# Optimization experiments

Measured on AMD Instinct MI355X. Metric: run time of the kernel, lower is better.

Reference implementation:

```python
import jax, jax.numpy as jnp
from jax import lax
import numpy as np

B, L, M, D = 128, 1024, 68, 2
H = 256          # lstm hidden
IN = M * D       # 136
FF1, FF2 = 256, 512
NLAYERS = 3


def _p(key, shape, scale=0.05):
    return (jax.random.normal(key, shape, dtype=jnp.float32) * scale)


def setup_inputs() -> dict:
    key = jax.random.key(0)
    ks = jax.random.split(key, 20)
    inp = {
        "x": jax.random.normal(ks[0], (B, L, M, D), dtype=jnp.float32),
        "length": jax.random.randint(ks[1], (B,), 1, L + 1, dtype=jnp.int32),
        # MLP: Linear(136,256) -> ReLU -> Linear(256,512) -> ReLU
        "W1": _p(ks[2], (FF1, IN)), "b1": _p(ks[3], (FF1,)),
        "W2": _p(ks[4], (FF2, FF1)), "b2": _p(ks[5], (FF2,)),
        # 3-layer LSTM(512 -> 256), torch gate order i,f,g,o
        "w_ih0": _p(ks[6], (4 * H, FF2)), "w_hh0": _p(ks[7], (4 * H, H)),
        "b_ih0": _p(ks[8], (4 * H,)), "b_hh0": _p(ks[9], (4 * H,)),
        "w_ih1": _p(ks[10], (4 * H, H)), "w_hh1": _p(ks[11], (4 * H, H)),
        "b_ih1": _p(ks[12], (4 * H,)), "b_hh1": _p(ks[13], (4 * H,)),
        "w_ih2": _p(ks[14], (4 * H, H)), "w_hh2": _p(ks[15], (4 * H, H)),
        "b_ih2": _p(ks[16], (4 * H,)), "b_hh2": _p(ks[17], (4 * H,)),
        # decision head Linear(256, 1)
        "Wd": _p(ks[18], (1, H)), "bd": _p(ks[19], (1,)),
    }
    return inp


def lstm_layer(x, w_ih, w_hh, b_ih, b_hh):
    # x: [B, L, Din] -> [B, L, H]; zero initial (h, c)
    b, l, _ = x.shape
    h = w_hh.shape[1]
    xg = jnp.einsum('bld,gd->blg', x, w_ih) + b_ih + b_hh  # [B,L,4H]
    xg = jnp.swapaxes(xg, 0, 1)  # [L,B,4H]

    def step(carry, xt):
        hh, cc = carry
        gates = xt + hh @ w_hh.T
        i, f, g, o = jnp.split(gates, 4, axis=-1)
        i = jax.nn.sigmoid(i)
        f = jax.nn.sigmoid(f)
        g = jnp.tanh(g)
        o = jax.nn.sigmoid(o)
        cc = f * cc + i * g
        hh = o * jnp.tanh(cc)
        return (hh, cc), hh

    init = (jnp.zeros((b, h), x.dtype), jnp.zeros((b, h), x.dtype))
    _, hs = lax.scan(step, init, xg)
    return jnp.swapaxes(hs, 0, 1)  # [B,L,H]


def reference(x, length, W1, b1, W2, b2,
              w_ih0, w_hh0, b_ih0, b_hh0,
              w_ih1, w_hh1, b_ih1, b_hh1,
              w_ih2, w_hh2, b_ih2, b_hh2,
              Wd, bd):
    b, l, m, d = x.shape
    feat = x.reshape(b, l, m * d)
    feat = jax.nn.relu(jnp.einsum('bld,od->blo', feat, W1) + b1)
    feat = jax.nn.relu(jnp.einsum('bld,od->blo', feat, W2) + b2)  # [B,L,512]
    h = lstm_layer(feat, w_ih0, w_hh0, b_ih0, b_hh0)
    h = lstm_layer(h, w_ih1, w_hh1, b_ih1, b_hh1)
    h = lstm_layer(h, w_ih2, w_hh2, b_ih2, b_hh2)  # [B,L,256]
    decision = jnp.einsum('blh,oh->blo', h, Wd)[..., 0] + bd[0]  # [B,L]
    # ragged mean over the first length[i] timesteps (AdaptiveAvgPool1d(1))
    mask = (jnp.arange(l)[None, :] < length[:, None]).astype(decision.dtype)
    out = jnp.sum(decision * mask, axis=1) / length.astype(decision.dtype)
    return out  # [B]
```

## Files before the change

### kernel.cpp

```cpp
#include <hip/hip_runtime.h>
#include <hip/hip_fp16.h>

#define TCH 256
#define NCH 4

typedef __attribute__((ext_vector_type(8))) _Float16 half8;
typedef __attribute__((ext_vector_type(2))) _Float16 half2v;
typedef __attribute__((ext_vector_type(4))) float floatx4;

__device__ __forceinline__ float dot2f(unsigned a, unsigned b, float c) {
#if __has_builtin(__builtin_amdgcn_fdot2)
  return __builtin_amdgcn_fdot2(__builtin_bit_cast(half2v, a),
                                __builtin_bit_cast(half2v, b), c, false);
#else
  __half2 x = __builtin_bit_cast(__half2, a);
  __half2 y = __builtin_bit_cast(__half2, b);
  c = fmaf(__half2float(x.x), __half2float(y.x), c);
  c = fmaf(__half2float(x.y), __half2float(y.y), c);
  return c;
#endif
}

template<bool AF32, bool RELUB>
__global__ __launch_bounds__(256, 2) void gemm_k(
    const void* __restrict__ Ab, const float* __restrict__ Bw,
    const float* __restrict__ bias, __half* __restrict__ C,
    const int* __restrict__ length, int K, int KT, int N, int arst, int t0)
{
  int b = blockIdx.x >> 1;
  int tloc0 = (blockIdx.x & 1) << 7;
  if (t0 + tloc0 >= length[b]) return;

  __shared__ half8 As[128][5];
  __shared__ half8 Bs[128][5];

  int tid = threadIdx.x;
  int wave = tid >> 6, lane = tid & 63;
  int wm = (wave & 1) << 6, wn = (wave >> 1) << 6;
  int quad = lane >> 4, sub = lane & 15;
  int n0 = blockIdx.y << 7;

  floatx4 acc[4][4];
#pragma unroll
  for (int i = 0; i < 4; ++i)
#pragma unroll
    for (int j = 0; j < 4; ++j)
#pragma unroll
      for (int e = 0; e < 4; ++e) acc[i][j][e] = 0.f;

  size_t arowbase = (size_t)b * arst + tloc0;

  for (int kt = 0; kt < KT; ++kt) {
    int k0 = kt << 5;
#pragma unroll
    for (int pass = 0; pass < 2; ++pass) {
      int idx = tid + (pass << 8);
      int r = idx >> 2, c8 = (idx & 3) << 3;
      int kb = k0 + c8;
      half8 v;
      if (AF32) {
        const float* src = (const float*)Ab + (arowbase + r) * K + kb;
        if (kb + 8 <= K) {
          float4 u0 = *(const float4*)(src);
          float4 u1 = *(const float4*)(src + 4);
          v[0] = (_Float16)u0.x; v[1] = (_Float16)u0.y; v[2] = (_Float16)u0.z; v[3] = (_Float16)u0.w;
          v[4] = (_Float16)u1.x; v[5] = (_Float16)u1.y; v[6] = (_Float16)u1.z; v[7] = (_Float16)u1.w;
        } else {
#pragma unroll
          for (int i = 0; i < 8; ++i) v[i] = (kb + i < K) ? (_Float16)src[i] : (_Float16)0.f;
        }
      } else {
        const __half* src = (const __half*)Ab + (arowbase + r) * K + kb;
        if (kb + 8 <= K) v = *(const half8*)src;
        else {
#pragma unroll
          for (int i = 0; i < 8; ++i) v[i] = (kb + i < K) ? *(const _Float16*)(src + i) : (_Float16)0.f;
        }
      }
      As[r][c8 >> 3] = v;
      const float* bsrc = Bw + (size_t)(n0 + r) * K + kb;
      half8 w;
      if (kb + 8 <= K) {
        float4 u0 = *(const float4*)(bsrc);
        float4 u1 = *(const float4*)(bsrc + 4);
        w[0] = (_Float16)u0.x; w[1] = (_Float16)u0.y; w[2] = (_Float16)u0.z; w[3] = (_Float16)u0.w;
        w[4] = (_Float16)u1.x; w[5] = (_Float16)u1.y; w[6] = (_Float16)u1.z; w[7] = (_Float16)u1.w;
      } else {
#pragma unroll
        for (int i = 0; i < 8; ++i) w[i] = (kb + i < K) ? (_Float16)bsrc[i] : (_Float16)0.f;
      }
      Bs[r][c8 >> 3] = w;
    }
    __syncthreads();
    half8 af[4], bf[4];
#pragma unroll
    for (int i = 0; i < 4; ++i) {
      af[i] = As[wm + (i << 4) + sub][quad];
      bf[i] = Bs[wn + (i << 4) + sub][quad];
    }
#pragma unroll
    for (int mt = 0; mt < 4; ++mt)
#pragma unroll
      for (int nt = 0; nt < 4; ++nt)
        acc[mt][nt] = __builtin_amdgcn_mfma_f32_16x16x32_f16(af[mt], bf[nt], acc[mt][nt], 0, 0, 0);
    __syncthreads();
  }
  size_t mrowbase = (size_t)blockIdx.x << 7;
#pragma unroll
  for (int nt = 0; nt < 4; ++nt) {
    int n = n0 + wn + (nt << 4) + sub;
    float bv = 0.f;
    if (RELUB) bv = bias[n];
#pragma unroll
    for (int mt = 0; mt < 4; ++mt) {
#pragma unroll
      for (int r4 = 0; r4 < 4; ++r4) {
        int m = wm + (mt << 4) + (quad << 2) + r4;
        float v = acc[mt][nt][r4] + bv;
        if (RELUB) v = fmaxf(v, 0.f);
        C[(mrowbase + m) * (size_t)N + n] = __float2half(v);
      }
    }
  }
}

__global__ __launch_bounds__(512, 2) void scan_k(
    const __half* __restrict__ xg, const float* __restrict__ whh,
    const float* __restrict__ bih, const float* __restrict__ bhh,
    __half* __restrict__ hout, unsigned* __restrict__ hstate,
    float* __restrict__ cstate, unsigned long long* __restrict__ exch,
    const int* __restrict__ length, int t0)
{
  int b = blockIdx.x >> 1, hf = blockIdx.x & 1;
  int len = length[b];
  int tend = min(t0 + TCH, len);
  if (t0 >= tend) return;

  int tid = threadIdx.x;
  int lane = tid & 63;
  int gate = tid >> 7, hl = tid & 127;
  int row = (gate << 8) + (hf << 7) + hl;

  __shared__ float gbuf[512];
  __shared__ unsigned short hbf[128];
  __shared__ unsigned opair[64];

  unsigned wp[128];
  {
    const float* wsrc = whh + (size_t)row * 256;
#pragma unroll
    for (int p2 = 0; p2 < 64; ++p2) {
      float4 f = *(const float4*)(wsrc + (p2 << 2));
      unsigned pk0 = ((unsigned)__half_as_ushort(__float2half(f.y)) << 16) | __half_as_ushort(__float2half(f.x));
      unsigned pk1 = ((unsigned)__half_as_ushort(__float2half(f.w)) << 16) | __half_as_ushort(__float2half(f.z));
      int p = p2 << 1;
      int pj0 = ((p >> 6) == hf) ? (p & 63) : (64 + (p & 63));
      int pa = p + 1;
      int pj1 = ((pa >> 6) == hf) ? (pa & 63) : (64 + (pa & 63));
      wp[pj0] = pk0;
      wp[pj1] = pk1;
    }
  }
  float biasr = bih[row] + bhh[row];

  unsigned hp0 = 0, hp1 = 0;
  float cv = 0.f;
  if (t0 > 0) {
    hp0 = hstate[(b << 7) + (hf << 6) + lane];
    hp1 = hstate[(b << 7) + ((1 - hf) << 6) + lane];
    if (tid < 128) cv = cstate[(b << 8) + (hf << 7) + tid];
  }

  const __half* xgp = xg + ((size_t)b * TCH) * 1024 + row;
  unsigned long long* exA = exch + ((((size_t)b << 1) | (size_t)hf) << 7);
  unsigned long long* exB = exch + ((((size_t)b << 1) | (size_t)(1 - hf)) << 7);

  for (int t = t0; t < tend; ++t) {
    float xgv = __half2float(xgp[(size_t)(t - t0) << 10]);
    float acc = biasr;
#pragma unroll
    for (int j = 0; j < 64; ++j)
      acc = dot2f(wp[j], (unsigned)__builtin_amdgcn_readlane(hp0, j), acc);
    if (t > t0) {
      const unsigned long long* pw = exB + ((t & 1) << 6) + lane;
      unsigned long long w = __hip_atomic_load(pw, __ATOMIC_RELAXED, __HIP_MEMORY_SCOPE_AGENT);
      while ((int)(unsigned)(w >> 32) != t) {
        __builtin_amdgcn_s_sleep(2);
        w = __hip_atomic_load(pw, __ATOMIC_RELAXED, __HIP_MEMORY_SCOPE_AGENT);
      }
      hp1 = (unsigned)w;
    }
#pragma unroll
    for (int j = 0; j < 64; ++j)
      acc = dot2f(wp[64 + j], (unsigned)__builtin_amdgcn_readlane(hp1, j), acc);
    acc += xgv;
    float gv = (gate == 2) ? tanhf(acc) : (1.f / (1.f + __expf(-acc)));
    gbuf[tid] = gv;
    __syncthreads();
    if (tid < 128) {
      float iv = gbuf[tid], fv = gbuf[128 + tid], gg = gbuf[256 + tid], ov = gbuf[384 + tid];
      cv = fv * cv + iv * gg;
      float hv = ov * tanhf(cv);
      __half hh = __float2half(hv);
      hout[(((size_t)b * TCH) + (t - t0)) * 256 + (hf << 7) + tid] = hh;
      hbf[tid] = __half_as_ushort(hh);
    }
    __syncthreads();
    if (tid < 64) {
      unsigned pr = ((unsigned)hbf[(tid << 1) + 1] << 16) | hbf[tid << 1];
      opair[tid] = pr;
      __hip_atomic_store(exA + (((t + 1) & 1) << 6) + tid,
                         ((unsigned long long)(unsigned)(t + 1) << 32) | (unsigned long long)pr,
                         __ATOMIC_RELAXED, __HIP_MEMORY_SCOPE_AGENT);
    }
    __syncthreads();
    hp0 = opair[lane];
  }
  if (tid < 64) hstate[(b << 7) + (hf << 6) + tid] = hp0;
  if (tid < 128) cstate[(b << 8) + (hf << 7) + tid] = cv;
}

__global__ __launch_bounds__(256, 2) void head_k(
    const __half* __restrict__ h2, const float* __restrict__ Wd,
    const float* __restrict__ bd, const int* __restrict__ length,
    float* __restrict__ dacc, float* __restrict__ out, int t0, int first, int last)
{
  int b = blockIdx.x, tid = threadIdx.x;
  int lane = tid & 63, wave = tid >> 6;
  int len = length[b];
  int tend = min(t0 + TCH, len);
  float4 w4 = *(const float4*)(Wd + (lane << 2));
  float wsum = 0.f;
  for (int t = t0 + wave; t < tend; t += 4) {
    const __half* hr = h2 + (((size_t)b * TCH) + (t - t0)) * 256 + (lane << 2);
    uint2 u = *(const uint2*)hr;
    __half2 p0 = __builtin_bit_cast(__half2, u.x);
    __half2 p1 = __builtin_bit_cast(__half2, u.y);
    float s = w4.x * __half2float(p0.x) + w4.y * __half2float(p0.y)
            + w4.z * __half2float(p1.x) + w4.w * __half2float(p1.y);
#pragma unroll
    for (int off = 32; off > 0; off >>= 1) s += __shfl_xor(s, off);
    wsum += s;
  }
  __shared__ float wred[4];
  if (lane == 0) wred[wave] = wsum;
  __syncthreads();
  if (tid == 0) {
    int cnt = tend - t0; if (cnt < 0) cnt = 0;
    float tot = wred[0] + wred[1] + wred[2] + wred[3] + bd[0] * (float)cnt;
    if (!first) tot += dacc[b];
    dacc[b] = tot;
    if (last) out[b] = tot / (float)len;
  }
}

extern "C" void kernel_launch(void* const* d_in, const int* in_sizes, int n_in,
                              void* d_out, int out_size, void* d_ws, size_t ws_size,
                              hipStream_t stream) {
  (void)in_sizes; (void)n_in; (void)out_size; (void)ws_size;
  const float* x    = (const float*)d_in[0];
  const int* length = (const int*)d_in[1];
  const float* W1   = (const float*)d_in[2];
  const float* b1   = (const float*)d_in[3];
  const float* W2   = (const float*)d_in[4];
  const float* b2   = (const float*)d_in[5];
  const float* wih[3] = {(const float*)d_in[6],  (const float*)d_in[10], (const float*)d_in[14]};
  const float* whh[3] = {(const float*)d_in[7],  (const float*)d_in[11], (const float*)d_in[15]};
  const float* bih[3] = {(const float*)d_in[8],  (const float*)d_in[12], (const float*)d_in[16]};
  const float* bhh[3] = {(const float*)d_in[9],  (const float*)d_in[13], (const float*)d_in[17]};
  const float* Wd   = (const float*)d_in[18];
  const float* bd   = (const float*)d_in[19];
  float* out = (float*)d_out;

  char* ws = (char*)d_ws;
  __half* XG    = (__half*)(ws);
  __half* FEAT1 = (__half*)(ws + 67108864);
  __half* FEAT2 = (__half*)(ws + 83886080);
  __half* HBUF  = (__half*)(ws + 117440512);
  unsigned* HST = (unsigned*)(ws + 134217728);
  float* CST    = (float*)(ws + 134217728 + 196608);
  unsigned long long* EXC = (unsigned long long*)(ws + 134217728 + 589824);
  float* DACC   = (float*)(ws + 134217728 + 589824 + 786432);

  for (int c = 0; c < NCH; ++c) {
    int t0 = c * TCH;
    gemm_k<true,  true ><<<dim3(256, 2), 256, 0, stream>>>(
        (const void*)(x + (size_t)t0 * 136), W1, b1, FEAT1, length, 136, 5, 256, 1024, t0);
    gemm_k<false, true ><<<dim3(256, 4), 256, 0, stream>>>(
        (const void*)FEAT1, W2, b2, FEAT2, length, 256, 8, 512, TCH, t0);
    gemm_k<false, false><<<dim3(256, 8), 256, 0, stream>>>(
        (const void*)FEAT2, wih[0], nullptr, XG, length, 512, 16, 1024, TCH, t0);
    scan_k<<<256, 512, 0, stream>>>(XG, whh[0], bih[0], bhh[0], HBUF,
                                    HST, CST, EXC, length, t0);
    gemm_k<false, false><<<dim3(256, 8), 256, 0, stream>>>(
        (const void*)HBUF, wih[1], nullptr, XG, length, 256, 8, 1024, TCH, t0);
    scan_k<<<256, 512, 0, stream>>>(XG, whh[1], bih[1], bhh[1], HBUF,
                                    HST + 16384, CST + 32768, EXC + 32768, length, t0);
    gemm_k<false, false><<<dim3(256, 8), 256, 0, stream>>>(
        (const void*)HBUF, wih[2], nullptr, XG, length, 256, 8, 1024, TCH, t0);
    scan_k<<<256, 512, 0, stream>>>(XG, whh[2], bih[2], bhh[2], HBUF,
                                    HST + 32768, CST + 65536, EXC + 65536, length, t0);
    head_k<<<128, 256, 0, stream>>>(HBUF, Wd, bd, length, DACC, out, t0, c == 0, c == NCH - 1);
  }
}
```

Before: 6.474 ms.

## Batch LSTM recurrence over 16 sequences per block using MFMA

Replaces the per-sequence scalar dot2 recurrence (two blocks per batch element, exchanging halves of h) with a kernel where groups of 16 batch rows are split across 8 blocks by hidden-column slice. Each step computes the recurrent matmul with 16x16x32 f16 MFMA. The full h vector is exchanged through tagged global slots that every block polls. This is meant to cut the serial per-step latency and the total block count. In exchange, each block now waits on 8 peer blocks per step and runs up to the longest sequence in its group. It also depends on all 64 blocks being co-resident to avoid deadlock.

After: 11.81 ms. 1.82x slower.

```diff
diff --git a/kernel.cpp b/kernel.cpp
--- a/kernel.cpp
+++ b/kernel.cpp
@@ -5,21 +5,7 @@
 #define NCH 4
 
 typedef __attribute__((ext_vector_type(8))) _Float16 half8;
-typedef __attribute__((ext_vector_type(2))) _Float16 half2v;
 typedef __attribute__((ext_vector_type(4))) float floatx4;
-
-__device__ __forceinline__ float dot2f(unsigned a, unsigned b, float c) {
-#if __has_builtin(__builtin_amdgcn_fdot2)
-  return __builtin_amdgcn_fdot2(__builtin_bit_cast(half2v, a),
-                                __builtin_bit_cast(half2v, b), c, false);
-#else
-  __half2 x = __builtin_bit_cast(__half2, a);
-  __half2 y = __builtin_bit_cast(__half2, b);
-  c = fmaf(__half2float(x.x), __half2float(y.x), c);
-  c = fmaf(__half2float(x.y), __half2float(y.y), c);
-  return c;
-#endif
-}
 
 template<bool AF32, bool RELUB>
 __global__ __launch_bounds__(256, 2) void gemm_k(
@@ -124,100 +110,132 @@
   }
 }
 
-__global__ __launch_bounds__(512, 2) void scan_k(
+__global__ __launch_bounds__(256, 2) void scan2_k(
     const __half* __restrict__ xg, const float* __restrict__ whh,
     const float* __restrict__ bih, const float* __restrict__ bhh,
-    __half* __restrict__ hout, unsigned* __restrict__ hstate,
-    float* __restrict__ cstate, unsigned long long* __restrict__ exch,
+    __half* __restrict__ hout, float* __restrict__ cstate,
+    unsigned long long* __restrict__ exch,
     const int* __restrict__ length, int t0)
 {
-  int b = blockIdx.x >> 1, hf = blockIdx.x & 1;
-  int len = length[b];
-  int tend = min(t0 + TCH, len);
+  const int g = blockIdx.x >> 3, s = blockIdx.x & 7;
+  const int b0 = g << 4;
+  int maxlen = 0;
+#pragma unroll
+  for (int i = 0; i < 16; ++i) maxlen = max(maxlen, length[b0 + i]);
+  const int tend = min(t0 + TCH, maxlen);
   if (t0 >= tend) return;
 
-  int tid = threadIdx.x;
-  int lane = tid & 63;
-  int gate = tid >> 7, hl = tid & 127;
-  int row = (gate << 8) + (hf << 7) + hl;
-
-  __shared__ float gbuf[512];
-  __shared__ unsigned short hbf[128];
-  __shared__ unsigned opair[64];
-
-  unsigned wp[128];
-  {
-    const float* wsrc = whh + (size_t)row * 256;
-#pragma unroll
-    for (int p2 = 0; p2 < 64; ++p2) {
-      float4 f = *(const float4*)(wsrc + (p2 << 2));
-      unsigned pk0 = ((unsigned)__half_as_ushort(__float2half(f.y)) << 16) | __half_as_ushort(__float2half(f.x));
-      unsigned pk1 = ((unsigned)__half_as_ushort(__float2half(f.w)) << 16) | __half_as_ushort(__float2half(f.z));
-      int p = p2 << 1;
-      int pj0 = ((p >> 6) == hf) ? (p & 63) : (64 + (p & 63));
-      int pa = p + 1;
-      int pj1 = ((pa >> 6) == hf) ? (pa & 63) : (64 + (pa & 63));
-      wp[pj0] = pk0;
-      wp[pj1] = pk1;
-    }
-  }
-  float biasr = bih[row] + bhh[row];
-
-  unsigned hp0 = 0, hp1 = 0;
-  float cv = 0.f;
-  if (t0 > 0) {
-    hp0 = hstate[(b << 7) + (hf << 6) + lane];
-    hp1 = hstate[(b << 7) + ((1 - hf) << 6) + lane];
-    if (tid < 128) cv = cstate[(b << 8) + (hf << 7) + tid];
-  }
-
-  const __half* xgp = xg + ((size_t)b * TCH) * 1024 + row;
-  unsigned long long* exA = exch + ((((size_t)b << 1) | (size_t)hf) << 7);
-  unsigned long long* exB = exch + ((((size_t)b << 1) | (size_t)(1 - hf)) << 7);
+  const int tid = threadIdx.x;
+  const int wave = tid >> 6, lane = tid & 63;
+  const int quad = lane >> 4, sub = lane & 15;
+
+  __shared__ __align__(16) __half h_lds[16][264];
+  __shared__ __align__(16) __half xgl[16][136];
+  __shared__ __align__(16) float gbuf[128][20];
+
+  half8 wB[8][2];
+  float bias2[2];
+#pragma unroll
+  for (int nt = 0; nt < 2; ++nt) {
+    int gcol = (wave << 8) + (s << 5) + (nt << 4) + sub;
+    bias2[nt] = bih[gcol] + bhh[gcol];
+#pragma unroll
+    for (int kt = 0; kt < 8; ++kt) {
+      const float* p = whh + (size_t)gcol * 256 + (kt << 5) + (quad << 3);
+      float4 a = *(const float4*)p;
+      float4 b4 = *(const float4*)(p + 4);
+      half8 v;
+      v[0] = (_Float16)a.x;  v[1] = (_Float16)a.y;  v[2] = (_Float16)a.z;  v[3] = (_Float16)a.w;
+      v[4] = (_Float16)b4.x; v[5] = (_Float16)b4.y; v[6] = (_Float16)b4.z; v[7] = (_Float16)b4.w;
+      wB[kt][nt] = v;
+    }
+  }
+
+  const int ub = tid >> 4, uc = tid & 15;
+  const int d0 = uc << 1;
+  float2 cc = make_float2(0.f, 0.f);
+  if (t0 > 0) cc = *(const float2*)&cstate[(size_t)((b0 + ub) << 8) + (s << 5) + d0];
+
+  if (t0 == 0) {
+    unsigned* hz = (unsigned*)&h_lds[0][0];
+    for (int i = tid; i < 16 * 132; i += 256) hz[i] = 0u;
+  }
+
+  const int sb = tid >> 4, sc = tid & 15;
+  const __half* xbase = xg + ((size_t)(b0 + sb) * TCH) * 1024
+                        + ((sc >> 2) << 8) + (s << 5) + ((sc & 3) << 3);
+  const unsigned long long* exrd = exch + ((size_t)(b0 + sb) << 1) * 128;
+  const size_t exwr_row = ((size_t)(b0 + ub) << 1);
+  const int widx = (s << 4) + uc;
 
   for (int t = t0; t < tend; ++t) {
-    float xgv = __half2float(xgp[(size_t)(t - t0) << 10]);
-    float acc = biasr;
-#pragma unroll
-    for (int j = 0; j < 64; ++j)
-      acc = dot2f(wp[j], (unsigned)__builtin_amdgcn_readlane(hp0, j), acc);
-    if (t > t0) {
-      const unsigned long long* pw = exB + ((t & 1) << 6) + lane;
-      unsigned long long w = __hip_atomic_load(pw, __ATOMIC_RELAXED, __HIP_MEMORY_SCOPE_AGENT);
-      while ((int)(unsigned)(w >> 32) != t) {
-        __builtin_amdgcn_s_sleep(2);
-        w = __hip_atomic_load(pw, __ATOMIC_RELAXED, __HIP_MEMORY_SCOPE_AGENT);
-      }
-      hp1 = (unsigned)w;
-    }
-#pragma unroll
-    for (int j = 0; j < 64; ++j)
-      acc = dot2f(wp[64 + j], (unsigned)__builtin_amdgcn_readlane(hp1, j), acc);
-    acc += xgv;
-    float gv = (gate == 2) ? tanhf(acc) : (1.f / (1.f + __expf(-acc)));
-    gbuf[tid] = gv;
+    const int tl = t - t0;
+    uint4 xv = *(const uint4*)(xbase + (size_t)tl * 1024);
+    if (t > 0) {
+      const unsigned long long* src = exrd + ((t & 1) << 7) + (sc << 3);
+      unsigned long long w[8];
+#pragma unroll
+      for (int j = 0; j < 8; ++j)
+        w[j] = __hip_atomic_load(src + j, __ATOMIC_RELAXED, __HIP_MEMORY_SCOPE_AGENT);
+      while (true) {
+        int bad = 0;
+#pragma unroll
+        for (int j = 0; j < 8; ++j) bad |= ((int)(unsigned)(w[j] >> 32) != t);
+        if (!bad) break;
+        __builtin_amdgcn_s_sleep(1);
+#pragma unroll
+        for (int j = 0; j < 8; ++j)
+          w[j] = __hip_atomic_load(src + j, __ATOMIC_RELAXED, __HIP_MEMORY_SCOPE_AGENT);
+      }
+      uint4 q0, q1;
+      q0.x = (unsigned)w[0]; q0.y = (unsigned)w[1]; q0.z = (unsigned)w[2]; q0.w = (unsigned)w[3];
+      q1.x = (unsigned)w[4]; q1.y = (unsigned)w[5]; q1.z = (unsigned)w[6]; q1.w = (unsigned)w[7];
+      *(uint4*)&h_lds[sb][(sc << 4)] = q0;
+      *(uint4*)&h_lds[sb][(sc << 4) + 8] = q1;
+    }
+    *(uint4*)&xgl[sb][((sc >> 2) << 5) + ((sc & 3) << 3)] = xv;
     __syncthreads();
-    if (tid < 128) {
-      float iv = gbuf[tid], fv = gbuf[128 + tid], gg = gbuf[256 + tid], ov = gbuf[384 + tid];
-      cv = fv * cv + iv * gg;
-      float hv = ov * tanhf(cv);
-      __half hh = __float2half(hv);
-      hout[(((size_t)b * TCH) + (t - t0)) * 256 + (hf << 7) + tid] = hh;
-      hbf[tid] = __half_as_ushort(hh);
+
+    floatx4 acc0 = {0.f, 0.f, 0.f, 0.f}, acc1 = {0.f, 0.f, 0.f, 0.f};
+#pragma unroll
+    for (int kt = 0; kt < 8; ++kt) {
+      half8 af = *(const half8*)&h_lds[sub][(kt << 5) + (quad << 3)];
+      acc0 = __builtin_amdgcn_mfma_f32_16x16x32_f16(af, wB[kt][0], acc0, 0, 0, 0);
+      acc1 = __builtin_amdgcn_mfma_f32_16x16x32_f16(af, wB[kt][1], acc1, 0, 0, 0);
+    }
+#pragma unroll
+    for (int nt = 0; nt < 2; ++nt) {
+      floatx4 av = nt ? acc1 : acc0;
+      float4 o;
+#pragma unroll
+      for (int r = 0; r < 4; ++r) {
+        float xvv = __half2float(xgl[(quad << 2) + r][(wave << 5) + (nt << 4) + sub]);
+        float pre = av[r] + xvv + bias2[nt];
+        float res;
+        if (wave == 2) res = tanhf(pre);
+        else           res = 1.f / (1.f + __expf(-pre));
+        (&o.x)[r] = res;
+      }
+      *(float4*)&gbuf[(wave << 5) + (nt << 4) + sub][quad << 2] = o;
     }
     __syncthreads();
-    if (tid < 64) {
-      unsigned pr = ((unsigned)hbf[(tid << 1) + 1] << 16) | hbf[tid << 1];
-      opair[tid] = pr;
-      __hip_atomic_store(exA + (((t + 1) & 1) << 6) + tid,
-                         ((unsigned long long)(unsigned)(t + 1) << 32) | (unsigned long long)pr,
-                         __ATOMIC_RELAXED, __HIP_MEMORY_SCOPE_AGENT);
-    }
-    __syncthreads();
-    hp0 = opair[lane];
-  }
-  if (tid < 64) hstate[(b << 7) + (hf << 6) + tid] = hp0;
-  if (tid < 128) cstate[(b << 8) + (hf << 7) + tid] = cv;
+
+    float iv0 = gbuf[d0][ub],      iv1 = gbuf[d0 + 1][ub];
+    float fv0 = gbuf[32 + d0][ub], fv1 = gbuf[33 + d0][ub];
+    float gv0 = gbuf[64 + d0][ub], gv1 = gbuf[65 + d0][ub];
+    float ov0 = gbuf[96 + d0][ub], ov1 = gbuf[97 + d0][ub];
+    cc.x = fv0 * cc.x + iv0 * gv0;
+    cc.y = fv1 * cc.y + iv1 * gv1;
+    float h0 = ov0 * tanhf(cc.x);
+    float h1 = ov1 * tanhf(cc.y);
+    unsigned pk = ((unsigned)__half_as_ushort(__float2half(h1)) << 16)
+                | (unsigned)__half_as_ushort(__float2half(h0));
+    *(unsigned*)&hout[(((size_t)(b0 + ub) * TCH) + tl) * 256 + (s << 5) + d0] = pk;
+    __hip_atomic_store(exch + (exwr_row + ((t + 1) & 1)) * 128 + widx,
+                       ((unsigned long long)(unsigned)(t + 1) << 32) | (unsigned long long)pk,
+                       __ATOMIC_RELAXED, __HIP_MEMORY_SCOPE_AGENT);
+  }
+  *(float2*)&cstate[(size_t)((b0 + ub) << 8) + (s << 5) + d0] = cc;
 }
 
 __global__ __launch_bounds__(256, 2) void head_k(
@@ -277,10 +295,9 @@
   __half* FEAT1 = (__half*)(ws + 67108864);
   __half* FEAT2 = (__half*)(ws + 83886080);
   __half* HBUF  = (__half*)(ws + 117440512);
-  unsigned* HST = (unsigned*)(ws + 134217728);
-  float* CST    = (float*)(ws + 134217728 + 196608);
-  unsigned long long* EXC = (unsigned long long*)(ws + 134217728 + 589824);
-  float* DACC   = (float*)(ws + 134217728 + 589824 + 786432);
+  unsigned long long* EXC = (unsigned long long*)(ws + 134217728);
+  float* CST    = (float*)(ws + 134217728 + 786432);
+  float* DACC   = (float*)(ws + 134217728 + 786432 + 393216);
 
   for (int c = 0; c < NCH; ++c) {
     int t0 = c * TCH;
@@ -290,16 +307,16 @@
         (const void*)FEAT1, W2, b2, FEAT2, length, 256, 8, 512, TCH, t0);
     gemm_k<false, false><<<dim3(256, 8), 256, 0, stream>>>(
         (const void*)FEAT2, wih[0], nullptr, XG, length, 512, 16, 1024, TCH, t0);
-    scan_k<<<256, 512, 0, stream>>>(XG, whh[0], bih[0], bhh[0], HBUF,
-                                    HST, CST, EXC, length, t0);
+    scan2_k<<<64, 256, 0, stream>>>(XG, whh[0], bih[0], bhh[0], HBUF,
+                                    CST, EXC, length, t0);
     gemm_k<false, false><<<dim3(256, 8), 256, 0, stream>>>(
         (const void*)HBUF, wih[1], nullptr, XG, length, 256, 8, 1024, TCH, t0);
-    scan_k<<<256, 512, 0, stream>>>(XG, whh[1], bih[1], bhh[1], HBUF,
-                                    HST + 16384, CST + 32768, EXC + 32768, length, t0);
+    scan2_k<<<64, 256, 0, stream>>>(XG, whh[1], bih[1], bhh[1], HBUF,
+                                    CST + 32768, EXC + 32768, length, t0);
     gemm_k<false, false><<<dim3(256, 8), 256, 0, stream>>>(
         (const void*)HBUF, wih[2], nullptr, XG, length, 256, 8, 1024, TCH, t0);
-    scan_k<<<256, 512, 0, stream>>>(XG, whh[2], bih[2], bhh[2], HBUF,
-                                    HST + 32768, CST + 65536, EXC + 65536, length, t0);
+    scan2_k<<<64, 256, 0, stream>>>(XG, whh[2], bih[2], bhh[2], HBUF,
+                                    CST + 65536, EXC + 65536, length, t0);
     head_k<<<128, 256, 0, stream>>>(HBUF, Wd, bd, length, DACC, out, t0, c == 0, c == NCH - 1);
   }
 }
```

## Run each LSTM scan in one workgroup per batch with weights split across registers and LDS

Applied to the files above, without the earlier changes.

The recurrent scan used two workgroups per batch element that exchanged half of the hidden state every step through global-memory atomics with spin-waiting. It now uses a single 512-thread workgroup per batch element. Each thread owns two gate rows, holding 96 packed fp16 weight pairs per row in registers and the remaining 32 in swizzled LDS (about 128KB of dynamic shared memory). A prep kernel packs the recurrent weights to fp16 once, the next step's xg is prefetched, and fast sigmoid/tanh via reciprocal replace tanhf. This removes the cross-workgroup synchronization, but it halves the number of workgroups and doubles the dot-product work per thread.

New measurement: 8.801 ms. 35.9% more time.

```diff
diff --git a/kernel.cpp b/kernel.cpp
--- a/kernel.cpp
+++ b/kernel.cpp
@@ -9,16 +9,14 @@
 typedef __attribute__((ext_vector_type(4))) float floatx4;
 
 __device__ __forceinline__ float dot2f(unsigned a, unsigned b, float c) {
-#if __has_builtin(__builtin_amdgcn_fdot2)
   return __builtin_amdgcn_fdot2(__builtin_bit_cast(half2v, a),
                                 __builtin_bit_cast(half2v, b), c, false);
-#else
-  __half2 x = __builtin_bit_cast(__half2, a);
-  __half2 y = __builtin_bit_cast(__half2, b);
-  c = fmaf(__half2float(x.x), __half2float(y.x), c);
-  c = fmaf(__half2float(x.y), __half2float(y.y), c);
-  return c;
-#endif
+}
+__device__ __forceinline__ float sigm_f(float x) {
+  return __frcp_rn(1.f + __expf(-x));
+}
+__device__ __forceinline__ float tanh_f(float x) {
+  return fmaf(2.f, __frcp_rn(1.f + __expf(-2.f * x)), -1.f);
 }
 
 template<bool AF32, bool RELUB>
@@ -124,100 +122,132 @@
   }
 }
 
-__global__ __launch_bounds__(512, 2) void scan_k(
-    const __half* __restrict__ xg, const float* __restrict__ whh,
+__global__ __launch_bounds__(256, 4) void prep_k(
+    const float* __restrict__ w0, const float* __restrict__ w1,
+    const float* __restrict__ w2, unsigned* __restrict__ wpk)
+{
+  int g = blockIdx.x * 256 + threadIdx.x;
+  int l = g >> 17, rem = g & 131071;
+  const float* src = (l == 0) ? w0 : (l == 1) ? w1 : w2;
+  float2 f = *(const float2*)(src + ((size_t)rem << 1));
+  wpk[g] = ((unsigned)__half_as_ushort(__float2half(f.y)) << 16)
+         | (unsigned)__half_as_ushort(__float2half(f.x));
+}
+
+__global__ __launch_bounds__(512, 2) void scan3_k(
+    const __half* __restrict__ xg, const unsigned* __restrict__ wpk,
     const float* __restrict__ bih, const float* __restrict__ bhh,
     __half* __restrict__ hout, unsigned* __restrict__ hstate,
-    float* __restrict__ cstate, unsigned long long* __restrict__ exch,
-    const int* __restrict__ length, int t0)
+    float* __restrict__ cstate, const int* __restrict__ length, int t0)
 {
-  int b = blockIdx.x >> 1, hf = blockIdx.x & 1;
-  int len = length[b];
-  int tend = min(t0 + TCH, len);
+  extern __shared__ char smem[];
+  unsigned* WL = (unsigned*)smem;
+  float* gbuf  = (float*)(smem + 131072);
+  __half* hh   = (__half*)(smem + 131072 + 4096);
+
+  const int b = blockIdx.x;
+  const int len = length[b];
+  const int tend = min(t0 + TCH, len);
   if (t0 >= tend) return;
 
-  int tid = threadIdx.x;
-  int lane = tid & 63;
-  int gate = tid >> 7, hl = tid & 127;
-  int row = (gate << 8) + (hf << 7) + hl;
-
-  __shared__ float gbuf[512];
-  __shared__ unsigned short hbf[128];
-  __shared__ unsigned opair[64];
-
-  unsigned wp[128];
+  const int tid = threadIdx.x;
+  const int lane = tid & 63;
+  const int r0 = tid, r1 = tid + 512;
+
+  unsigned w0[96], w1[96];
   {
-    const float* wsrc = whh + (size_t)row * 256;
-#pragma unroll
-    for (int p2 = 0; p2 < 64; ++p2) {
-      float4 f = *(const float4*)(wsrc + (p2 << 2));
-      unsigned pk0 = ((unsigned)__half_as_ushort(__float2half(f.y)) << 16) | __half_as_ushort(__float2half(f.x));
-      unsigned pk1 = ((unsigned)__half_as_ushort(__float2half(f.w)) << 16) | __half_as_ushort(__float2half(f.z));
-      int p = p2 << 1;
-      int pj0 = ((p >> 6) == hf) ? (p & 63) : (64 + (p & 63));
-      int pa = p + 1;
-      int pj1 = ((pa >> 6) == hf) ? (pa & 63) : (64 + (pa & 63));
-      wp[pj0] = pk0;
-      wp[pj1] = pk1;
-    }
-  }
-  float biasr = bih[row] + bhh[row];
+    const uint4* p0 = (const uint4*)(wpk + ((size_t)r0 << 7));
+    const uint4* p1 = (const uint4*)(wpk + ((size_t)r1 << 7));
+#pragma unroll
+    for (int i = 0; i < 24; ++i) {
+      uint4 a = p0[i];
+      w0[4*i] = a.x; w0[4*i+1] = a.y; w0[4*i+2] = a.z; w0[4*i+3] = a.w;
+      uint4 c = p1[i];
+      w1[4*i] = c.x; w1[4*i+1] = c.y; w1[4*i+2] = c.z; w1[4*i+3] = c.w;
+    }
+#pragma unroll
+    for (int c = 0; c < 8; ++c) {
+      uint4 a = p0[24 + c];
+      *(uint4*)&WL[(r0 << 5) + ((c ^ (r0 & 7)) << 2)] = a;
+      uint4 d = p1[24 + c];
+      *(uint4*)&WL[(r1 << 5) + ((c ^ (r1 & 7)) << 2)] = d;
+    }
+  }
+  const float bias0 = bih[r0] + bhh[r0];
+  const float bias1 = bih[r1] + bhh[r1];
 
   unsigned hp0 = 0, hp1 = 0;
   float cv = 0.f;
   if (t0 > 0) {
-    hp0 = hstate[(b << 7) + (hf << 6) + lane];
-    hp1 = hstate[(b << 7) + ((1 - hf) << 6) + lane];
-    if (tid < 128) cv = cstate[(b << 8) + (hf << 7) + tid];
-  }
-
-  const __half* xgp = xg + ((size_t)b * TCH) * 1024 + row;
-  unsigned long long* exA = exch + ((((size_t)b << 1) | (size_t)hf) << 7);
-  unsigned long long* exB = exch + ((((size_t)b << 1) | (size_t)(1 - hf)) << 7);
+    hp0 = hstate[(b << 7) + lane];
+    hp1 = hstate[(b << 7) + 64 + lane];
+    if (tid < 256) cv = cstate[(b << 8) + tid];
+  }
+  __syncthreads();
+
+  const __half* xgb = xg + (((size_t)b * TCH) << 10) + tid;
+  float xv0 = __half2float(xgb[0]);
+  float xv1 = __half2float(xgb[512]);
 
   for (int t = t0; t < tend; ++t) {
-    float xgv = __half2float(xgp[(size_t)(t - t0) << 10]);
-    float acc = biasr;
-#pragma unroll
-    for (int j = 0; j < 64; ++j)
-      acc = dot2f(wp[j], (unsigned)__builtin_amdgcn_readlane(hp0, j), acc);
-    if (t > t0) {
-      const unsigned long long* pw = exB + ((t & 1) << 6) + lane;
-      unsigned long long w = __hip_atomic_load(pw, __ATOMIC_RELAXED, __HIP_MEMORY_SCOPE_AGENT);
-      while ((int)(unsigned)(w >> 32) != t) {
-        __builtin_amdgcn_s_sleep(2);
-        w = __hip_atomic_load(pw, __ATOMIC_RELAXED, __HIP_MEMORY_SCOPE_AGENT);
-      }
-      hp1 = (unsigned)w;
-    }
-#pragma unroll
-    for (int j = 0; j < 64; ++j)
-      acc = dot2f(wp[64 + j], (unsigned)__builtin_amdgcn_readlane(hp1, j), acc);
-    acc += xgv;
-    float gv = (gate == 2) ? tanhf(acc) : (1.f / (1.f + __expf(-acc)));
-    gbuf[tid] = gv;
+    const int tl = t - t0;
+    const int tln = min(tl + 1, TCH - 1);
+    __half nx0 = xgb[(size_t)tln << 10];
+    __half nx1 = xgb[((size_t)tln << 10) + 512];
+
+    float a00 = 0.f, a01 = 0.f, a10 = 0.f, a11 = 0.f;
+    uint4 q0[2], q1[2];
+    q0[0] = *(const uint4*)&WL[(r0 << 5) + ((0 ^ (r0 & 7)) << 2)];
+    q1[0] = *(const uint4*)&WL[(r1 << 5) + ((0 ^ (r1 & 7)) << 2)];
+    q0[1] = *(const uint4*)&WL[(r0 << 5) + ((1 ^ (r0 & 7)) << 2)];
+    q1[1] = *(const uint4*)&WL[(r1 << 5) + ((1 ^ (r1 & 7)) << 2)];
+#pragma unroll
+    for (int s = 0; s < 8; ++s) {
+#pragma unroll
+      for (int j = 0; j < 12; ++j) {
+        const int p = s * 12 + j;
+        unsigned rl = (unsigned)__builtin_amdgcn_readlane(
+            (p < 64) ? (int)hp0 : (int)hp1, p & 63);
+        if (j & 1) { a01 = dot2f(w0[p], rl, a01); a11 = dot2f(w1[p], rl, a11); }
+        else       { a00 = dot2f(w0[p], rl, a00); a10 = dot2f(w1[p], rl, a10); }
+      }
+      uint4 c0 = q0[s & 1], c1 = q1[s & 1];
+      if (s < 6) {
+        q0[s & 1] = *(const uint4*)&WL[(r0 << 5) + (((s + 2) ^ (r0 & 7)) << 2)];
+        q1[s & 1] = *(const uint4*)&WL[(r1 << 5) + (((s + 2) ^ (r1 & 7)) << 2)];
+      }
+#pragma unroll
+      for (int j = 0; j < 4; ++j) {
+        unsigned rl = (unsigned)__builtin_amdgcn_readlane((int)hp1, 32 + s * 4 + j);
+        a01 = dot2f((&c0.x)[j], rl, a01);
+        a11 = dot2f((&c1.x)[j], rl, a11);
+      }
+    }
+    float pre0 = a00 + a01 + xv0 + bias0;
+    float pre1 = a10 + a11 + xv1 + bias1;
+    float g0 = sigm_f(pre0);
+    float g1 = (tid < 256) ? tanh_f(pre1) : sigm_f(pre1);
+    gbuf[r0] = g0;
+    gbuf[r1] = g1;
     __syncthreads();
-    if (tid < 128) {
-      float iv = gbuf[tid], fv = gbuf[128 + tid], gg = gbuf[256 + tid], ov = gbuf[384 + tid];
-      cv = fv * cv + iv * gg;
-      float hv = ov * tanhf(cv);
-      __half hh = __float2half(hv);
-      hout[(((size_t)b * TCH) + (t - t0)) * 256 + (hf << 7) + tid] = hh;
-      hbf[tid] = __half_as_ushort(hh);
+    if (tid < 256) {
+      float iv = gbuf[tid], fv = gbuf[256 + tid];
+      float gv = gbuf[512 + tid], ov = gbuf[768 + tid];
+      cv = fv * cv + iv * gv;
+      float hv = ov * tanh_f(cv);
+      __half hx = __float2half(hv);
+      hh[tid] = hx;
+      hout[(((size_t)b * TCH) + tl) * 256 + tid] = hx;
     }
     __syncthreads();
-    if (tid < 64) {
-      unsigned pr = ((unsigned)hbf[(tid << 1) + 1] << 16) | hbf[tid << 1];
-      opair[tid] = pr;
-      __hip_atomic_store(exA + (((t + 1) & 1) << 6) + tid,
-                         ((unsigned long long)(unsigned)(t + 1) << 32) | (unsigned long long)pr,
-                         __ATOMIC_RELAXED, __HIP_MEMORY_SCOPE_AGENT);
-    }
-    __syncthreads();
-    hp0 = opair[lane];
-  }
-  if (tid < 64) hstate[(b << 7) + (hf << 6) + tid] = hp0;
-  if (tid < 128) cstate[(b << 8) + (hf << 7) + tid] = cv;
+    hp0 = ((const unsigned*)hh)[lane];
+    hp1 = ((const unsigned*)hh)[64 + lane];
+    xv0 = __half2float(nx0);
+    xv1 = __half2float(nx1);
+  }
+  if (tid < 64)       hstate[(b << 7) + tid] = hp0;
+  else if (tid < 128) hstate[(b << 7) + tid] = hp1;
+  if (tid < 256) cstate[(b << 8) + tid] = cv;
 }
 
 __global__ __launch_bounds__(256, 2) void head_k(
@@ -277,10 +307,16 @@
   __half* FEAT1 = (__half*)(ws + 67108864);
   __half* FEAT2 = (__half*)(ws + 83886080);
   __half* HBUF  = (__half*)(ws + 117440512);
-  unsigned* HST = (unsigned*)(ws + 134217728);
-  float* CST    = (float*)(ws + 134217728 + 196608);
-  unsigned long long* EXC = (unsigned long long*)(ws + 134217728 + 589824);
-  float* DACC   = (float*)(ws + 134217728 + 589824 + 786432);
+  unsigned* WPK = (unsigned*)(ws + 134217728);
+  float* CST    = (float*)(ws + 134217728 + 1572864);
+  unsigned* HST = (unsigned*)(ws + 134217728 + 1572864 + 393216);
+  float* DACC   = (float*)(ws + 134217728 + 1572864 + 393216 + 196608);
+
+  (void)hipFuncSetAttribute((const void*)scan3_k,
+      hipFuncAttributeMaxDynamicSharedMemorySize, 136192);
+  const int SMEM = 131072 + 4096 + 512;
+
+  prep_k<<<1536, 256, 0, stream>>>(whh[0], whh[1], whh[2], WPK);
 
   for (int c = 0; c < NCH; ++c) {
     int t0 = c * TCH;
@@ -290,16 +326,16 @@
         (const void*)FEAT1, W2, b2, FEAT2, length, 256, 8, 512, TCH, t0);
     gemm_k<false, false><<<dim3(256, 8), 256, 0, stream>>>(
         (const void*)FEAT2, wih[0], nullptr, XG, length, 512, 16, 1024, TCH, t0);
-    scan_k<<<256, 512, 0, stream>>>(XG, whh[0], bih[0], bhh[0], HBUF,
-                                    HST, CST, EXC, length, t0);
+    scan3_k<<<128, 512, SMEM, stream>>>(XG, WPK, bih[0], bhh[0], HBUF,
+                                        HST, CST, length, t0);
     gemm_k<false, false><<<dim3(256, 8), 256, 0, stream>>>(
         (const void*)HBUF, wih[1], nullptr, XG, length, 256, 8, 1024, TCH, t0);
-    scan_k<<<256, 512, 0, stream>>>(XG, whh[1], bih[1], bhh[1], HBUF,
-                                    HST + 16384, CST + 32768, EXC + 32768, length, t0);
+    scan3_k<<<128, 512, SMEM, stream>>>(XG, WPK + 131072, bih[1], bhh[1], HBUF,
+                                        HST + 16384, CST + 32768, length, t0);
     gemm_k<false, false><<<dim3(256, 8), 256, 0, stream>>>(
         (const void*)HBUF, wih[2], nullptr, XG, length, 256, 8, 1024, TCH, t0);
-    scan_k<<<256, 512, 0, stream>>>(XG, whh[2], bih[2], bhh[2], HBUF,
-                                    HST + 32768, CST + 65536, EXC + 65536, length, t0);
+    scan3_k<<<128, 512, SMEM, stream>>>(XG, WPK + 262144, bih[2], bhh[2], HBUF,
+                                        HST + 32768, CST + 65536, length, t0);
     head_k<<<128, 256, 0, stream>>>(HBUF, Wd, bd, length, DACC, out, t0, c == 0, c == NCH - 1);
   }
 }
```
